# Optimization experiments

Measured on AMD Instinct MI355X. Metric: run time of the kernel, lower is better.

The kernel has to match this reference:

```python
import jax, jax.numpy as jnp
import numpy as np

B, V, H, NT, K_CD = 4096, 1024, 1024, 2, 10
L1_REG, L2_REG = 1e-5, 1e-4


def setup_inputs() -> dict:
    key = jax.random.key(0)
    ks = jax.random.split(key, 10)
    v0 = jax.random.bernoulli(ks[0], 0.5, (B, V)).astype(jnp.float32)
    # two distinct non-trivial (non-Z) sites per sample, one in each half
    tau0 = jax.random.randint(ks[1], (B,), 0, V // 2)
    tau1 = V // 2 + jax.random.randint(ks[2], (B,), 0, V // 2)
    tau_idx = jnp.stack([tau0, tau1], axis=1).astype(jnp.int32)
    basis_choice = jax.random.randint(ks[3], (B, NT), 1, 3).astype(jnp.int32)  # X=1 or Y=2
    basis_ids = jnp.zeros((B, V), jnp.int32)
    basis_ids = basis_ids.at[jnp.arange(B)[:, None], tau_idx].set(basis_choice)
    s = 1.0 / np.sqrt(2.0)
    un = np.zeros((3, 2, 2, 2), np.float32)  # [basis, row, col, re/im]
    un[0, :, :, 0] = np.eye(2)                              # Z: identity
    un[1, :, :, 0] = s * np.array([[1, 1], [1, -1]])        # X: Hadamard
    un[2, :, :, 0] = s * np.array([[1, 0], [1, 0]])         # Y: K gate, real
    un[2, :, :, 1] = s * np.array([[0, -1], [0, 1]])        # Y: K gate, imag
    unitaries = jnp.asarray(un)
    weights_amp = jax.random.normal(ks[4], (H, V), jnp.float32) / np.sqrt(V)
    weights_phase = 0.01 * jax.random.normal(ks[5], (H, V), jnp.float32)
    visible_bias_amp = 0.01 * jax.random.normal(ks[6], (V,), jnp.float32)
    hidden_bias_amp = 0.01 * jax.random.normal(ks[7], (H,), jnp.float32)
    visible_bias_phase = 0.01 * jax.random.normal(ks[8], (V,), jnp.float32)
    hidden_bias_phase = 0.01 * jax.random.normal(ks[9], (H,), jnp.float32)
    return {"v0": v0, "basis_ids": basis_ids, "tau_idx": tau_idx, "unitaries": unitaries,
            "weights_amp": weights_amp, "visible_bias_amp": visible_bias_amp,
            "hidden_bias_amp": hidden_bias_amp, "weights_phase": weights_phase,
            "visible_bias_phase": visible_bias_phase, "hidden_bias_phase": hidden_bias_phase,
            "k": K_CD}


def _forward(v0, unitaries, weights_amp, visible_bias_amp, hidden_bias_amp,
             weights_phase, visible_bias_phase, hidden_bias_phase,
             basis_ids, tau_idx, k):
    Bsz, Vn = v0.shape
    NTn = tau_idx.shape[1]
    C = 2 ** NTn
    # all 2^NT assignments of the rotated (tau) sites -> [C, NT]
    S = jnp.asarray(np.array([[(c >> (NTn - 1 - t)) & 1 for t in range(NTn)]
                              for c in range(C)], np.int32))
    U = (unitaries[..., 0] + 1j * unitaries[..., 1]).astype(jnp.complex64)  # [3,2,2]
    b_tau = jnp.take_along_axis(basis_ids, tau_idx, axis=1)                 # [B,NT]
    v0_tau = jnp.take_along_axis(v0, tau_idx, axis=1).astype(jnp.int32)     # [B,NT]
    # product over tau sites of unitary elements U_b[v0_j, s_j] -> [B,C]
    Uelem = U[b_tau[:, None, :], v0_tau[:, None, :], S[None, :, :]]
    wU = jnp.prod(Uelem, axis=-1)
    # v' = v0 with tau sites replaced by each assignment s -> [B,C,V]
    onehot = jax.nn.one_hot(tau_idx, Vn, dtype=v0.dtype)                    # [B,NT,V]
    mask = onehot.sum(1)
    vp = v0[:, None, :] * (1.0 - mask[:, None, :]) \
         + jnp.einsum('btv,ct->bcv', onehot, S.astype(v0.dtype))
    # unnormalized wavefunction psi(v') = sqrt(p_amp(v')) * exp(i*log(p_phase(v'))/2)
    pre_amp = jnp.einsum('bcv,hv->bch', vp, weights_amp) + hidden_bias_amp
    pre_ph = jnp.einsum('bcv,hv->bch', vp, weights_phase) + hidden_bias_phase
    log_amp = 0.5 * (vp @ visible_bias_amp + jax.nn.softplus(pre_amp).sum(-1))  # [B,C]
    theta = 0.5 * (vp @ visible_bias_phase + jax.nn.softplus(pre_ph).sum(-1))
    # per-sample shift cancels exactly in A/B; keeps exp() in fp32 range
    log_amp = log_amp - jax.lax.stop_gradient(log_amp.max(axis=1, keepdims=True))
    psi = (jnp.exp(log_amp) * (jnp.cos(theta) + 1j * jnp.sin(theta))).astype(jnp.complex64)
    w = wU * psi                                   # [B,C] complex
    coef = w / w.sum(axis=1, keepdims=True)        # A/B weighting per sample
    sig_amp = jax.nn.sigmoid(pre_amp)
    sig_ph = jax.nn.sigmoid(pre_ph)
    inv_b = 1.0 / Bsz
    Lw_amp = jnp.einsum('bc,bch,bcv->hv', coef, sig_amp, vp) * inv_b
    Lw_ph = jnp.einsum('bc,bch,bcv->hv', coef, sig_ph, vp) * inv_b
    Lvb = jnp.einsum('bc,bcv->v', coef, vp) * inv_b
    Lhb_amp = jnp.einsum('bc,bch->h', coef, sig_amp) * inv_b
    Lhb_ph = jnp.einsum('bc,bch->h', coef, sig_ph) * inv_b
    # amplitude params take Re(L) (negated positive phase); phase params take Im(L)
    g_w_amp = -jnp.real(Lw_amp)
    g_vb_amp = -jnp.real(Lvb)
    g_hb_amp = -jnp.real(Lhb_amp)
    g_w_ph = jnp.imag(Lw_ph)
    g_vb_ph = jnp.imag(Lvb)
    g_hb_ph = jnp.imag(Lhb_ph)
    # ---- CD-k Gibbs negative phase (amplitude RBM only) ----
    base_key = jax.random.key(1234)
    def gibbs_step(i, v):
        kh = jax.random.fold_in(base_key, 2 * i)
        kv = jax.random.fold_in(base_key, 2 * i + 1)
        ph = jax.nn.sigmoid(v @ weights_amp.T + hidden_bias_amp)
        h = (jax.random.uniform(kh, ph.shape) < ph).astype(v.dtype)
        pv = jax.nn.sigmoid(h @ weights_amp + visible_bias_amp)
        return (jax.random.uniform(kv, pv.shape) < pv).astype(v.dtype)
    vk = jax.lax.stop_gradient(jax.lax.fori_loop(0, k, gibbs_step, v0))
    sig_k = jax.nn.sigmoid(vk @ weights_amp.T + hidden_bias_amp)
    g_w_amp = g_w_amp + jnp.einsum('bh,bv->hv', sig_k, vk) * inv_b
    g_vb_amp = g_vb_amp + vk.mean(0)
    g_hb_amp = g_hb_amp + sig_k.mean(0)
    # ---- L1/L2 regularization on weight gradients ----
    g_w_amp = g_w_amp + L2_REG * weights_amp + L1_REG * jnp.sign(weights_amp)
    g_w_ph = g_w_ph + L2_REG * weights_phase + L1_REG * jnp.sign(weights_phase)
    return (g_w_amp, g_vb_amp, g_hb_amp, g_w_ph, g_vb_ph, g_hb_ph)


def reference(v0, basis_ids, tau_idx, unitaries, weights_amp, visible_bias_amp,
              hidden_bias_amp, weights_phase, visible_bias_phase, hidden_bias_phase, k):
    return _forward(v0, unitaries, weights_amp, visible_bias_amp, hidden_bias_amp,
                    weights_phase, visible_bias_phase, hidden_bias_phase,
                    basis_ids, tau_idx, k)
```

## Files before the change

### kernel.cpp

```cpp
#include <hip/hip_runtime.h>
#include <cstdint>
#include <cstddef>

#define BSZ 4096
#define VN  1024
#define HN  1024
#define NSTEPS 10

static constexpr float INVB = 1.0f / 4096.0f;
static constexpr float L1R  = 1e-5f;
static constexpr float L2R  = 1e-4f;

typedef __attribute__((ext_vector_type(8)))  __bf16        bf16x8;
typedef __attribute__((ext_vector_type(8)))  unsigned short ushort8;
typedef __attribute__((ext_vector_type(16))) float          f32x16;

__device__ static inline unsigned short f2bf(float x){
  unsigned u = __float_as_uint(x);
  unsigned r = (u + 0x7FFFu + ((u >> 16) & 1u)) >> 16;
  return (unsigned short)r;
}
__device__ static inline float bf2f(unsigned short s){
  return __uint_as_float(((unsigned)s) << 16);
}

__device__ __forceinline__ void gload16(const void* g, void* l){
  __builtin_amdgcn_global_load_lds(
      (__attribute__((address_space(1))) void*)(g),
      (__attribute__((address_space(3))) void*)(l),
      16, 0, 0);
}

#define TFR(x0,x1,r) { x0 += x1; x1 = ((x1)<<(r))|((x1)>>(32-(r))); x1 ^= x0; }

__host__ __device__ static inline void tf2x32(unsigned k0, unsigned k1,
                                              unsigned x0, unsigned x1,
                                              unsigned &o0, unsigned &o1)
{
  const unsigned ks2 = k0 ^ k1 ^ 0x1BD11BDAu;
  x0 += k0; x1 += k1;
  TFR(x0,x1,13) TFR(x0,x1,15) TFR(x0,x1,26) TFR(x0,x1,6)
  x0 += k1; x1 += ks2 + 1u;
  TFR(x0,x1,17) TFR(x0,x1,29) TFR(x0,x1,16) TFR(x0,x1,24)
  x0 += ks2; x1 += k0 + 2u;
  TFR(x0,x1,13) TFR(x0,x1,15) TFR(x0,x1,26) TFR(x0,x1,6)
  x0 += k0; x1 += k1 + 3u;
  TFR(x0,x1,17) TFR(x0,x1,29) TFR(x0,x1,16) TFR(x0,x1,24)
  x0 += k1; x1 += ks2 + 4u;
  TFR(x0,x1,13) TFR(x0,x1,15) TFR(x0,x1,26) TFR(x0,x1,6)
  x0 += ks2; x1 += k0 + 5u;
  o0 = x0; o1 = x1;
}

__device__ static inline float tf_uniform(unsigned k0, unsigned k1, unsigned e)
{
  unsigned o0, o1; tf2x32(k0, k1, 0u, e, o0, o1);
  const unsigned r = o0 ^ o1;
  return __uint_as_float((r >> 9) | 0x3f800000u) - 1.0f;
}

__device__ static inline float sigmoidf(float x){ return 1.0f/(1.0f+expf(-x)); }

__global__ void zero_kernel(float* __restrict__ p, int n){
  int i = blockIdx.x*256 + threadIdx.x;
  if (i < n) p[i] = 0.0f;
}

__global__ void prep_kernel(const float* __restrict__ v0,
                            const int* __restrict__ tau,
                            float* __restrict__ v0m,
                            float* __restrict__ v_cur,
                            unsigned short* __restrict__ v0m_bf,
                            unsigned short* __restrict__ v_bf)
{
  int i = blockIdx.x*256 + threadIdx.x;
  int b = i >> 10;
  int v = i & (VN-1);
  float x = v0[i];
  v_cur[i] = x;
  v_bf[i]  = f2bf(x);
  int t0 = tau[2*b], t1 = tau[2*b+1];
  float xm = (v==t0 || v==t1) ? 0.0f : x;
  v0m[i]    = xm;
  v0m_bf[i] = f2bf(xm);
}

__global__ void transpose_kernel(const float* __restrict__ Wa,
                                 const float* __restrict__ Wp,
                                 float* __restrict__ WTa,
                                 float* __restrict__ WTp)
{
  __shared__ float tile[32][33];
  const float* in = blockIdx.z ? Wp : Wa;
  float* out      = blockIdx.z ? WTp : WTa;
  int x  = blockIdx.x*32 + threadIdx.x;
  int y0 = blockIdx.y*32;
  for (int j = threadIdx.y; j < 32; j += 8)
    tile[j][threadIdx.x] = in[(size_t)(y0+j)*VN + x];
  __syncthreads();
  int xo  = y0 + threadIdx.x;
  int yo0 = blockIdx.x*32;
  for (int j = threadIdx.y; j < 32; j += 8)
    out[(size_t)(yo0+j)*HN + xo] = tile[threadIdx.x][j];
}

__global__ void transpose_to_bf(const float* __restrict__ X,
                                unsigned short* __restrict__ XT,
                                float* __restrict__ cs)
{
  __shared__ float tile[32][33];
  const int tx = threadIdx.x, ty = threadIdx.y;
  int x  = blockIdx.x*32 + tx;
  int y0 = blockIdx.y*32;
  for (int j = ty; j < 32; j += 8)
    tile[j][tx] = X[(size_t)(y0+j)*1024 + x];
  __syncthreads();
  int xo  = y0 + tx;
  int yo0 = blockIdx.x*32;
  for (int j = ty; j < 32; j += 8)
    XT[(size_t)(yo0+j)*BSZ + xo] = f2bf(tile[tx][j]);
  float s = tile[ty][tx] + tile[ty+8][tx] + tile[ty+16][tx] + tile[ty+24][tx];
  __syncthreads();
  tile[ty][tx] = s;
  __syncthreads();
  if (ty == 0){
    float t = 0.f;
    #pragma unroll
    for (int j = 0; j < 8; j++) t += tile[j][tx];
    atomicAdd(cs + x, t);
  }
}

__global__ void split_weights(const float* __restrict__ Wa,
                              const float* __restrict__ Wp,
                              const float* __restrict__ WTa,
                              unsigned short* __restrict__ WaHi,
                              unsigned short* __restrict__ WaLo,
                              unsigned short* __restrict__ WpHi,
                              unsigned short* __restrict__ WpLo,
                              unsigned short* __restrict__ WaTHi,
                              unsigned short* __restrict__ WaTLo)
{
  size_t i = (size_t)blockIdx.x*256 + threadIdx.x;
  float w = Wa[i];  unsigned short h = f2bf(w);
  WaHi[i] = h;  WaLo[i] = f2bf(w - bf2f(h));
  w = Wp[i];  h = f2bf(w);
  WpHi[i] = h;  WpLo[i] = f2bf(w - bf2f(h));
  w = WTa[i]; h = f2bf(w);
  WaTHi[i] = h; WaTLo[i] = f2bf(w - bf2f(h));
}

#define GM 64
#define GN 64
#define GK 64

template<int MODE>
__global__ __launch_bounds__(256) void mfma_nt(
    const unsigned short* __restrict__ A,
    const unsigned short* __restrict__ Bhi,
    const unsigned short* __restrict__ Blo,
    const float* __restrict__ bias,
    unsigned short* __restrict__ out_bf,
    float* __restrict__ out_f,
    unsigned key0, unsigned key1)
{
  constexpr int K = 1024;
  constexpr int N = 1024;
  __shared__ ushort8 ldsA [GM*8];
  __shared__ ushort8 ldsBh[GN*8];
  __shared__ ushort8 ldsBl[GN*8];

  const int orig = blockIdx.x + gridDim.x * blockIdx.y;
  const int swz  = (orig & 7) * 128 + (orig >> 3);
  const int bx   = swz & 15, by = swz >> 4;
  const int m0   = by*GM, n0 = bx*GN;

  const int tid  = threadIdx.x;
  const int lane = tid & 63, w = tid >> 6;
  const int wm = w >> 1, wn = w & 1;
  const int l31 = lane & 31, hi = lane >> 5;
  const int rsub = lane >> 3;
  const int cch  = lane & 7;

  f32x16 acc = {};

  const int arow = wm*32 + l31;
  const int brow = wn*32 + l31;
  const int aswz = arow & 7;
  const int bswz = brow & 7;
  const int aidx = arow*8;
  const int bidx = brow*8;

  for (int kt = 0; kt < K/GK; ++kt){
    __syncthreads();
    const size_t kbase = (size_t)kt*GK;
    #pragma unroll
    for (int p = 0; p < 2; p++){
      const int row  = p*32 + w*8 + rsub;
      const int csrc = cch ^ (row & 7);
      gload16(A   + (size_t)(m0+row)*K + kbase + csrc*8, &ldsA [(p*32 + w*8)*8]);
      gload16(Bhi + (size_t)(n0+row)*K + kbase + csrc*8, &ldsBh[(p*32 + w*8)*8]);
      gload16(Blo + (size_t)(n0+row)*K + kbase + csrc*8, &ldsBl[(p*32 + w*8)*8]);
    }
    __syncthreads();

    #pragma unroll
    for (int s = 0; s < 4; s++){
      const int c = s*2 + hi;
      const bf16x8 a  = __builtin_bit_cast(bf16x8, ldsA [aidx + (c ^ aswz)]);
      const bf16x8 bh = __builtin_bit_cast(bf16x8, ldsBh[bidx + (c ^ bswz)]);
      const bf16x8 bl = __builtin_bit_cast(bf16x8, ldsBl[bidx + (c ^ bswz)]);
      acc = __builtin_amdgcn_mfma_f32_32x32x16_bf16(a, bh, acc, 0, 0, 0);
      acc = __builtin_amdgcn_mfma_f32_32x32x16_bf16(a, bl, acc, 0, 0, 0);
    }
  }

  const int n  = n0 + wn*32 + l31;
  const float bv = bias[n];
  const int mbase = m0 + wm*32 + 4*hi;
  #pragma unroll
  for (int r = 0; r < 16; r++){
    const int m = mbase + (r&3) + 8*(r>>2);
    const float pre = acc[r] + bv;
    const size_t o = (size_t)m*N + n;
    if constexpr (MODE == 0 || MODE == 1){
      const float p = sigmoidf(pre);
      const float u = tf_uniform(key0, key1, (unsigned)(m*N + n));
      out_bf[o] = (u < p) ? (unsigned short)0x3F80 : (unsigned short)0;
      if constexpr (MODE == 1) out_f[o] = (u < p) ? 1.0f : 0.0f;
    } else if constexpr (MODE == 2){
      out_f[o] = sigmoidf(pre);
    } else {
      out_f[o] = pre;
    }
  }
}

template<int NPROD>
__global__ __launch_bounds__(256) void mfma_grad(
    const unsigned short* __restrict__ A1,
    const unsigned short* __restrict__ B1,
    const unsigned short* __restrict__ A2,
    const unsigned short* __restrict__ B2,
    const float* __restrict__ Wreg,
    float* __restrict__ gW)
{
  constexpr int K = BSZ;
  __shared__ ushort8 lA1[64*8];
  __shared__ ushort8 lB1[64*8];
  __shared__ ushort8 lA2[(NPROD==2)?64*8:1];
  __shared__ ushort8 lB2[(NPROD==2)?64*8:1];

  const int tid  = threadIdx.x;
  const int m0   = blockIdx.y*64, n0 = blockIdx.x*64;
  const int lane = tid & 63, w = tid >> 6;
  const int wm = w >> 1, wn = w & 1;
  const int l31 = lane & 31, hi = lane >> 5;
  const int srow = tid >> 3, sc = tid & 7;

  f32x16 acc1a = {}, acc1b = {}, acc2a = {}, acc2b = {};

  const int arow = wm*32 + l31;
  const int brow = wn*32 + l31;
  const int aswz = arow & 7, bswz = brow & 7;
  const int aidx = arow*8,  bidx = brow*8;

  for (int kt = 0; kt < K/64; ++kt){
    __syncthreads();
    const size_t kof = (size_t)kt*64 + sc*8;
    #pragma unroll
    for (int p = 0; p < 2; p++){
      const int row = p*32 + srow;
      const int c = sc ^ (row & 7);
      lA1[row*8 + c] = *(const ushort8*)(A1 + (size_t)(m0+row)*K + kof);
      lB1[row*8 + c] = *(const ushort8*)(B1 + (size_t)(n0+row)*K + kof);
      if constexpr (NPROD==2){
        lA2[row*8 + c] = *(const ushort8*)(A2 + (size_t)(m0+row)*K + kof);
        lB2[row*8 + c] = *(const ushort8*)(B2 + (size_t)(n0+row)*K + kof);
      }
    }
    __syncthreads();
    #pragma unroll
    for (int s = 0; s < 4; s++){
      const int c = s*2 + hi;
      const bf16x8 a1 = __builtin_bit_cast(bf16x8, lA1[aidx + (c ^ aswz)]);
      const bf16x8 b1 = __builtin_bit_cast(bf16x8, lB1[bidx + (c ^ bswz)]);
      if (s & 1) acc1b = __builtin_amdgcn_mfma_f32_32x32x16_bf16(a1, b1, acc1b, 0,0,0);
      else       acc1a = __builtin_amdgcn_mfma_f32_32x32x16_bf16(a1, b1, acc1a, 0,0,0);
      if constexpr (NPROD==2){
        const bf16x8 a2 = __builtin_bit_cast(bf16x8, lA2[aidx + (c ^ aswz)]);
        const bf16x8 b2 = __builtin_bit_cast(bf16x8, lB2[bidx + (c ^ bswz)]);
        if (s & 1) acc2b = __builtin_amdgcn_mfma_f32_32x32x16_bf16(a2, b2, acc2b, 0,0,0);
        else       acc2a = __builtin_amdgcn_mfma_f32_32x32x16_bf16(a2, b2, acc2a, 0,0,0);
      }
    }
  }

  const int n = n0 + wn*32 + l31;
  #pragma unroll
  for (int r = 0; r < 16; r++){
    const int m = m0 + wm*32 + 4*hi + (r&3) + 8*(r>>2);
    const size_t o = (size_t)m*VN + n;
    float val;
    if constexpr (NPROD==2)
      val = INVB*((acc1a[r]+acc1b[r]) - (acc2a[r]+acc2b[r]));
    else
      val = INVB*(acc1a[r]+acc1b[r]);
    const float wv = Wreg[o];
    const float sg = (wv>0.f)?1.f:((wv<0.f)?-1.f:0.f);
    gW[o] += val + L2R*wv + L1R*sg;
  }
}

__global__ __launch_bounds__(256) void coef_ramp_kernel(
    const float* __restrict__ pre0a, const float* __restrict__ pre0p,
    const float* __restrict__ WTa,   const float* __restrict__ WTp,
    const float* __restrict__ v0,
    const float* __restrict__ vbA,   const float* __restrict__ vbP,
    const int*   __restrict__ tau,   const int*   __restrict__ basis,
    const float* __restrict__ unit,
    float* __restrict__ coefRe, float* __restrict__ coefIm,
    float* __restrict__ tmpA,   float* __restrict__ tmpP,
    float* __restrict__ Ramp,   float* __restrict__ Iph)
{
  const int b = blockIdx.x;
  const int t = threadIdx.x;
  const int t0 = tau[2*b], t1 = tau[2*b+1];

  float d[6] = {0,0,0,0,0,0};
  float st_sa[4], st_sp[4], st_a0[4], st_a1[4], st_p0[4], st_p1[4];

  #pragma unroll
  for (int i = 0; i < 4; i++){
    const int h = t + i*256;
    const float pa = pre0a[(size_t)b*HN + h], pp = pre0p[(size_t)b*HN + h];
    const float a0 = WTa[(size_t)t0*HN + h], a1 = WTa[(size_t)t1*HN + h];
    const float p0 = WTp[(size_t)t0*HN + h], p1 = WTp[(size_t)t1*HN + h];
    const float sa  = sigmoidf(pa);
    const float sp  = sigmoidf(pp);
    const float s1a = sa*(1.f-sa), ta2 = 1.f-2.f*sa, s2a = s1a*ta2;
    const float s1p = sp*(1.f-sp), tp2 = 1.f-2.f*sp, s2p = s1p*tp2;
    const float a01 = a0 + a1, p01 = p0 + p1;
    d[0] += a1 *(sa + a1 *(0.5f*s1a + 0.16666667f*a1 *s2a));
    d[1] += a0 *(sa + a0 *(0.5f*s1a + 0.16666667f*a0 *s2a));
    d[2] += a01*(sa + a01*(0.5f*s1a + 0.16666667f*a01*s2a));
    d[3] += p1 *(sp + p1 *(0.5f*s1p + 0.16666667f*p1 *s2p));
    d[4] += p0 *(sp + p0 *(0.5f*s1p + 0.16666667f*p0 *s2p));
    d[5] += p01*(sp + p01*(0.5f*s1p + 0.16666667f*p01*s2p));
    st_sa[i]=sa; st_sp[i]=sp; st_a0[i]=a0; st_a1[i]=a1; st_p0[i]=p0; st_p1[i]=p1;
  }

  __shared__ float red[6][4];
  __shared__ float lcr[4], lci[4];
  const int lane = t & 63, wv = t >> 6;
  #pragma unroll
  for (int i=0;i<6;i++){
    float x = d[i];
    for (int off=32; off>0; off>>=1) x += __shfl_down(x, off);
    if (lane==0) red[i][wv] = x;
  }
  __syncthreads();

  if (t==0){
    double ds[6];
    #pragma unroll
    for (int i=0;i<6;i++)
      ds[i] = (double)red[i][0]+red[i][1]+red[i][2]+red[i][3];

    const int bas0 = basis[(size_t)b*VN + t0], bas1 = basis[(size_t)b*VN + t1];
    const int x0 = (int)v0[(size_t)b*VN + t0], x1 = (int)v0[(size_t)b*VN + t1];
    const double A0 = vbA[t0], A1 = vbA[t1], P0 = vbP[t0], P1 = vbP[t1];

    double la[4], th[4];
    la[0]=0.0;                th[0]=0.0;
    la[1]=0.5*(A1+ds[0]);     th[1]=0.5*(P1+ds[3]);
    la[2]=0.5*(A0+ds[1]);     th[2]=0.5*(P0+ds[4]);
    la[3]=0.5*(A0+A1+ds[2]);  th[3]=0.5*(P0+P1+ds[5]);

    double wR[4], wI[4], sr=0.0, si=0.0;
    #pragma unroll
    for (int c=0;c<4;c++){
      const int s0 = (c>>1)&1, s1 = c&1;
      const float* u0 = unit + (((size_t)bas0*2 + x0)*2 + s0)*2;
      const float* u1 = unit + (((size_t)bas1*2 + x1)*2 + s1)*2;
      const double uR = (double)u0[0]*u1[0] - (double)u0[1]*u1[1];
      const double uI = (double)u0[0]*u1[1] + (double)u0[1]*u1[0];
      const double e  = exp(la[c]);
      const double cs = cos(th[c]), sn = sin(th[c]);
      wR[c] = e*(uR*cs - uI*sn);
      wI[c] = e*(uR*sn + uI*cs);
      sr += wR[c]; si += wI[c];
    }
    const double dd = sr*sr + si*si;
    #pragma unroll
    for (int c=0;c<4;c++){
      const float cr = (float)((wR[c]*sr + wI[c]*si)/dd);
      const float ci = (float)((wI[c]*sr - wR[c]*si)/dd);
      coefRe[b*4+c] = cr;  coefIm[b*4+c] = ci;
      lcr[c] = cr;         lci[c] = ci;
    }
    atomicAdd(tmpA + t0, lcr[2]+lcr[3]);
    atomicAdd(tmpA + t1, lcr[1]+lcr[3]);
    atomicAdd(tmpP + t0, lci[2]+lci[3]);
    atomicAdd(tmpP + t1, lci[1]+lci[3]);
  }
  __syncthreads();

  const float cr0=lcr[0], cr1=lcr[1], cr2=lcr[2], cr3=lcr[3];
  const float ci0=lci[0], ci1=lci[1], ci2=lci[2], ci3=lci[3];

  #pragma unroll
  for (int i = 0; i < 4; i++){
    const int h = t + i*256;
    const float sa = st_sa[i], sp = st_sp[i];
    const float a0 = st_a0[i], a1 = st_a1[i], p0 = st_p0[i], p1 = st_p1[i];
    const float s1a = sa*(1.f-sa), ta2 = 1.f-2.f*sa;
    const float s2a = s1a*ta2,     s3a = s1a*(ta2*ta2 - 2.f*s1a);
    const float s1p = sp*(1.f-sp), tp2 = 1.f-2.f*sp;
    const float s2p = s1p*tp2,     s3p = s1p*(tp2*tp2 - 2.f*s1p);
    const float a01 = a0 + a1, p01 = p0 + p1;
    const float sgA1 = sa + a1 *(s1a + a1 *(0.5f*s2a + 0.16666667f*a1 *s3a));
    const float sgA0 = sa + a0 *(s1a + a0 *(0.5f*s2a + 0.16666667f*a0 *s3a));
    const float sgA01= sa + a01*(s1a + a01*(0.5f*s2a + 0.16666667f*a01*s3a));
    const float sgP1 = sp + p1 *(s1p + p1 *(0.5f*s2p + 0.16666667f*p1 *s3p));
    const float sgP0 = sp + p0 *(s1p + p0 *(0.5f*s2p + 0.16666667f*p0 *s3p));
    const float sgP01= sp + p01*(s1p + p01*(0.5f*s2p + 0.16666667f*p01*s3p));
    Ramp[(size_t)b*HN + h] = cr0*sa + cr1*sgA1 + cr2*sgA0 + cr3*sgA01;
    Iph [(size_t)b*HN + h] = ci0*sp + ci1*sgP1 + ci2*sgP0 + ci3*sgP01;
  }
}

__global__ void csr_count(const int* __restrict__ tau, int* __restrict__ cnt){
  int b = blockIdx.x*256 + threadIdx.x;
  atomicAdd(cnt + tau[2*b],   1);
  atomicAdd(cnt + tau[2*b+1], 1);
}

__global__ __launch_bounds__(1024) void csr_scan(const int* __restrict__ cnt,
                                                 int* __restrict__ off,
                                                 int* __restrict__ cur){
  __shared__ int s[1024];
  const int t = threadIdx.x;
  s[t] = cnt[t];
  __syncthreads();
  for (int d=1; d<1024; d<<=1){
    int v = 0;
    if (t >= d) v = s[t-d];
    __syncthreads();
    s[t] += v;
    __syncthreads();
  }
  const int excl = (t==0) ? 0 : s[t-1];
  off[t] = excl; cur[t] = excl;
}

__global__ void csr_fill(const int* __restrict__ tau, int* __restrict__ cur,
                         int* __restrict__ list){
  int b = blockIdx.x*256 + threadIdx.x;
  int p0 = atomicAdd(cur + tau[2*b],   1); list[p0] = b;
  int p1 = atomicAdd(cur + tau[2*b+1], 1); list[p1] = b;
}

__global__ __launch_bounds__(256) void scatter_v2(
    const float* __restrict__ pre0a, const float* __restrict__ pre0p,
    const float* __restrict__ WTa,   const float* __restrict__ WTp,
    const int*   __restrict__ tau,
    const float* __restrict__ coefRe, const float* __restrict__ coefIm,
    const int* __restrict__ cnt, const int* __restrict__ off,
    const int* __restrict__ list,
    float* __restrict__ gWa, float* __restrict__ gWp)
{
  const int v = blockIdx.x;
  const int n = cnt[v];
  if (n == 0) return;
  const int o = off[v];
  const int c_lo = (v < 512) ? 2 : 1;
  const bool lo_half = (v < 512);

  const int h = blockIdx.y*256 + threadIdx.x;
  const float av = WTa[(size_t)v*HN + h];
  const float pv = WTp[(size_t)v*HN + h];
  float accA = 0.f, accP = 0.f;
  int e = o;
  for (; e + 2 <= o + n; e += 2){
    const int b0 = list[e], b1 = list[e+1];
    const int ot0 = lo_half ? tau[2*b0+1] : tau[2*b0];
    const int ot1 = lo_half ? tau[2*b1+1] : tau[2*b1];
    const float aoA0 = WTa[(size_t)ot0*HN + h], aoA1 = WTa[(size_t)ot1*HN + h];
    const float aoP0 = WTp[(size_t)ot0*HN + h], aoP1 = WTp[(size_t)ot1*HN + h];
    const float pa0 = pre0a[(size_t)b0*HN + h], pa1 = pre0a[(size_t)b1*HN + h];
    const float pp0 = pre0p[(size_t)b0*HN + h], pp1 = pre0p[(size_t)b1*HN + h];
    const float crl0 = coefRe[b0*4 + c_lo], cr30 = coefRe[b0*4 + 3];
    const float cil0 = coefIm[b0*4 + c_lo], ci30 = coefIm[b0*4 + 3];
    const float crl1 = coefRe[b1*4 + c_lo], cr31 = coefRe[b1*4 + 3];
    const float cil1 = coefIm[b1*4 + c_lo], ci31 = coefIm[b1*4 + 3];
    accA += crl0*sigmoidf(pa0 + av) + cr30*sigmoidf(pa0 + av + aoA0);
    accP += cil0*sigmoidf(pp0 + pv) + ci30*sigmoidf(pp0 + pv + aoP0);
    accA += crl1*sigmoidf(pa1 + av) + cr31*sigmoidf(pa1 + av + aoA1);
    accP += cil1*sigmoidf(pp1 + pv) + ci31*sigmoidf(pp1 + pv + aoP1);
  }
  if (e < o + n){
    const int b0 = list[e];
    const int ot0 = lo_half ? tau[2*b0+1] : tau[2*b0];
    const float aoA0 = WTa[(size_t)ot0*HN + h];
    const float aoP0 = WTp[(size_t)ot0*HN + h];
    const float pa0 = pre0a[(size_t)b0*HN + h];
    const float pp0 = pre0p[(size_t)b0*HN + h];
    const float crl0 = coefRe[b0*4 + c_lo], cr30 = coefRe[b0*4 + 3];
    const float cil0 = coefIm[b0*4 + c_lo], ci30 = coefIm[b0*4 + 3];
    accA += crl0*sigmoidf(pa0 + av) + cr30*sigmoidf(pa0 + av + aoA0);
    accP += cil0*sigmoidf(pp0 + pv) + ci30*sigmoidf(pp0 + pv + aoP0);
  }
  gWa[(size_t)h*VN + v] += -INVB*accA;
  gWp[(size_t)h*VN + v] +=  INVB*accP;
}

__global__ void final_small(
    const float* __restrict__ csV0m, const float* __restrict__ csVk,
    const float* __restrict__ csSigk, const float* __restrict__ csRamp,
    const float* __restrict__ csIph,
    const float* __restrict__ tmpA, const float* __restrict__ tmpP,
    float* __restrict__ gVa, float* __restrict__ gHa,
    float* __restrict__ gVp, float* __restrict__ gHp)
{
  const int j = blockIdx.x*256 + threadIdx.x;
  if (j < VN){
    gVa[j] = INVB*(csVk[j] - csV0m[j] - tmpA[j]);
    gVp[j] = INVB*tmpP[j];
  }
  if (j < HN){
    gHa[j] = INVB*(csSigk[j] - csRamp[j]);
    gHp[j] = INVB*csIph[j];
  }
}

extern "C" void kernel_launch(void* const* d_in, const int* in_sizes, int n_in,
                              void* d_out, int out_size, void* d_ws, size_t ws_size,
                              hipStream_t stream)
{
  const float* v0    = (const float*)d_in[0];
  const int*   basis = (const int*)  d_in[1];
  const int*   tau   = (const int*)  d_in[2];
  const float* unit  = (const float*)d_in[3];
  const float* Wa    = (const float*)d_in[4];
  const float* vbA   = (const float*)d_in[5];
  const float* hbA   = (const float*)d_in[6];
  const float* Wp    = (const float*)d_in[7];
  const float* vbP   = (const float*)d_in[8];
  const float* hbP   = (const float*)d_in[9];

  float* ws    = (float*)d_ws;
  float* v0m   = ws;  ws += (size_t)BSZ*VN;
  float* v_cur = ws;  ws += (size_t)BSZ*VN;
  float* h_buf = ws;  ws += (size_t)BSZ*HN;
  float* WTa   = ws;  ws += (size_t)VN*HN;
  float* WTp   = ws;  ws += (size_t)VN*HN;
  float* pre0a = ws;  ws += (size_t)BSZ*HN;
  float* pre0p = ws;  ws += (size_t)BSZ*HN;
  float* Ramp  = ws;  ws += (size_t)BSZ*HN;
  float* Iph   = ws;  ws += (size_t)BSZ*HN;
  float* coefRe= ws;  ws += (size_t)BSZ*4;
  float* coefIm= ws;  ws += (size_t)BSZ*4;
  float* tmpA  = ws;  ws += VN;
  float* tmpP  = ws;  ws += VN;
  float* csV0m = ws;  ws += VN;
  float* csVk  = ws;  ws += VN;
  float* csSigk= ws;  ws += HN;
  float* csRamp= ws;  ws += HN;
  float* csIph = ws;  ws += HN;
  int*   csrCnt = (int*)ws;  ws += VN;
  int*   csrOff = (int*)ws;  ws += VN;
  int*   csrCur = (int*)ws;  ws += VN;
  int*   csrLst = (int*)ws;  ws += 2*BSZ;
  unsigned short* v_bf    = (unsigned short*)ws;  ws += (size_t)BSZ*VN/2;
  unsigned short* h_bf    = (unsigned short*)ws;  ws += (size_t)BSZ*HN/2;
  unsigned short* v0m_bf  = (unsigned short*)ws;  ws += (size_t)BSZ*VN/2;
  unsigned short* WaHi    = (unsigned short*)ws;  ws += (size_t)HN*VN/2;
  unsigned short* WaLo    = (unsigned short*)ws;  ws += (size_t)HN*VN/2;
  unsigned short* WpHi    = (unsigned short*)ws;  ws += (size_t)HN*VN/2;
  unsigned short* WpLo    = (unsigned short*)ws;  ws += (size_t)HN*VN/2;
  unsigned short* WaTHi   = (unsigned short*)ws;  ws += (size_t)HN*VN/2;
  unsigned short* WaTLo   = (unsigned short*)ws;  ws += (size_t)HN*VN/2;

  float* sig_k = h_buf;
  unsigned short* v0mT  = (unsigned short*)pre0a;
  unsigned short* vkT   = v0mT + (size_t)VN*BSZ;
  unsigned short* RampT = (unsigned short*)pre0p;
  unsigned short* IphT  = RampT + (size_t)HN*BSZ;
  unsigned short* sigkT = (unsigned short*)WTa;

  float* out = (float*)d_out;
  float* gWa = out;
  float* gVa = gWa + (size_t)HN*VN;
  float* gHa = gVa + VN;
  float* gWp = gHa + HN;
  float* gVp = gWp + (size_t)HN*VN;
  float* gHp = gVp + VN;

  const dim3 gemm_grid(VN/GN, BSZ/GM);
  const dim3 tr_grid(1024/32, BSZ/32);
  const dim3 tr_blk(32, 8);

  zero_kernel<<<dim3(40), 256, 0, stream>>>(tmpA, 10*1024);
  zero_kernel<<<dim3((out_size+255)/256), 256, 0, stream>>>(out, out_size);
  prep_kernel<<<dim3(BSZ*VN/256), 256, 0, stream>>>(v0, tau, v0m, v_cur, v0m_bf, v_bf);
  transpose_kernel<<<dim3(VN/32, HN/32, 2), dim3(32,8), 0, stream>>>(Wa, Wp, WTa, WTp);
  split_weights<<<dim3(HN*VN/256), 256, 0, stream>>>(
      Wa, Wp, WTa, WaHi, WaLo, WpHi, WpLo, WaTHi, WaTLo);

  mfma_nt<3><<<gemm_grid, 256, 0, stream>>>(
      v0m_bf, WaHi, WaLo, hbA, nullptr, pre0a, 0u, 0u);
  mfma_nt<3><<<gemm_grid, 256, 0, stream>>>(
      v0m_bf, WpHi, WpLo, hbP, nullptr, pre0p, 0u, 0u);
  coef_ramp_kernel<<<dim3(BSZ), 256, 0, stream>>>(
      pre0a, pre0p, WTa, WTp, v0, vbA, vbP, tau, basis, unit,
      coefRe, coefIm, tmpA, tmpP, Ramp, Iph);

  csr_count<<<dim3(BSZ/256), 256, 0, stream>>>(tau, csrCnt);
  csr_scan <<<dim3(1), 1024, 0, stream>>>(csrCnt, csrOff, csrCur);
  csr_fill <<<dim3(BSZ/256), 256, 0, stream>>>(tau, csrCur, csrLst);
  scatter_v2<<<dim3(VN, 4), 256, 0, stream>>>(
      pre0a, pre0p, WTa, WTp, tau, coefRe, coefIm,
      csrCnt, csrOff, csrLst, gWa, gWp);

  for (int i = 0; i < NSTEPS; i++){
    unsigned kh0, kh1, kv0, kv1;
    tf2x32(0u, 1234u, 0u, (unsigned)(2*i),   kh0, kh1);
    tf2x32(0u, 1234u, 0u, (unsigned)(2*i+1), kv0, kv1);
    mfma_nt<0><<<gemm_grid, 256, 0, stream>>>(
        v_bf, WaHi, WaLo, hbA, h_bf, nullptr, kh0, kh1);
    if (i < NSTEPS-1)
      mfma_nt<0><<<gemm_grid, 256, 0, stream>>>(
          h_bf, WaTHi, WaTLo, vbA, v_bf, nullptr, kv0, kv1);
    else
      mfma_nt<1><<<gemm_grid, 256, 0, stream>>>(
          h_bf, WaTHi, WaTLo, vbA, v_bf, v_cur, kv0, kv1);
  }
  mfma_nt<2><<<gemm_grid, 256, 0, stream>>>(
      v_bf, WaHi, WaLo, hbA, nullptr, sig_k, 0u, 0u);

  transpose_to_bf<<<tr_grid, tr_blk, 0, stream>>>(v0m,   v0mT,  csV0m);
  transpose_to_bf<<<tr_grid, tr_blk, 0, stream>>>(v_cur, vkT,   csVk);
  transpose_to_bf<<<tr_grid, tr_blk, 0, stream>>>(Ramp,  RampT, csRamp);
  transpose_to_bf<<<tr_grid, tr_blk, 0, stream>>>(Iph,   IphT,  csIph);
  transpose_to_bf<<<tr_grid, tr_blk, 0, stream>>>(sig_k, sigkT, csSigk);

  mfma_grad<2><<<dim3(VN/64, HN/64), 256, 0, stream>>>(
      sigkT, vkT, RampT, v0mT, Wa, gWa);
  mfma_grad<1><<<dim3(VN/64, HN/64), 256, 0, stream>>>(
      IphT, v0mT, nullptr, nullptr, Wp, gWp);

  final_small<<<dim3(4), 256, 0, stream>>>(
      csV0m, csVk, csSigk, csRamp, csIph, tmpA, tmpP, gVa, gHa, gVp, gHp);
}
```

Measured before the change: 965.4 us.

## Enlarge Gibbs GEMM tiles to 128x128 with 2x2 MFMA blocking per wave

The forward GEMM kernel's block tile grows from 64x64 to 128x128. Each wave now computes a 64x64 sub-tile with four 32x32 accumulators, so every A and B fragment read from LDS is reused twice. The grid swizzle and epilogue loops are rewritten to match the larger tile. The aim is to cut global and LDS traffic per FLOP in the Gibbs sampling GEMMs. The costs are fewer blocks (256 instead of 1024), which can hurt occupancy and load balance, plus higher register pressure from 64 accumulator floats per lane.

```diff
diff --git a/kernel.cpp b/kernel.cpp
--- a/kernel.cpp
+++ b/kernel.cpp
@@ -150,8 +150,8 @@
   WaTHi[i] = h; WaTLo[i] = f2bf(w - bf2f(h));
 }
 
-#define GM 64
-#define GN 64
+#define GM 128
+#define GN 128
 #define GK 64
 
 template<int MODE>
@@ -171,8 +171,8 @@
   __shared__ ushort8 ldsBl[GN*8];
 
   const int orig = blockIdx.x + gridDim.x * blockIdx.y;
-  const int swz  = (orig & 7) * 128 + (orig >> 3);
-  const int bx   = swz & 15, by = swz >> 4;
+  const int swz  = (orig & 7) * 32 + (orig >> 3);
+  const int bx   = swz & 7, by = swz >> 3;
   const int m0   = by*GM, n0 = bx*GN;
 
   const int tid  = threadIdx.x;
@@ -182,20 +182,20 @@
   const int rsub = lane >> 3;
   const int cch  = lane & 7;
 
-  f32x16 acc = {};
-
-  const int arow = wm*32 + l31;
-  const int brow = wn*32 + l31;
-  const int aswz = arow & 7;
-  const int bswz = brow & 7;
-  const int aidx = arow*8;
-  const int bidx = brow*8;
+  f32x16 acc00 = {}, acc01 = {}, acc10 = {}, acc11 = {};
+
+  const int arow0 = wm*64 + l31;
+  const int brow0 = wn*64 + l31;
+  const int aswz  = arow0 & 7;
+  const int bswz  = brow0 & 7;
+  const int aidx0 = arow0*8,      aidx1 = (arow0+32)*8;
+  const int bidx0 = brow0*8,      bidx1 = (brow0+32)*8;
 
   for (int kt = 0; kt < K/GK; ++kt){
     __syncthreads();
     const size_t kbase = (size_t)kt*GK;
     #pragma unroll
-    for (int p = 0; p < 2; p++){
+    for (int p = 0; p < 4; p++){
       const int row  = p*32 + w*8 + rsub;
       const int csrc = cch ^ (row & 7);
       gload16(A   + (size_t)(m0+row)*K + kbase + csrc*8, &ldsA [(p*32 + w*8)*8]);
@@ -207,31 +207,47 @@
     #pragma unroll
     for (int s = 0; s < 4; s++){
       const int c = s*2 + hi;
-      const bf16x8 a  = __builtin_bit_cast(bf16x8, ldsA [aidx + (c ^ aswz)]);
-      const bf16x8 bh = __builtin_bit_cast(bf16x8, ldsBh[bidx + (c ^ bswz)]);
-      const bf16x8 bl = __builtin_bit_cast(bf16x8, ldsBl[bidx + (c ^ bswz)]);
-      acc = __builtin_amdgcn_mfma_f32_32x32x16_bf16(a, bh, acc, 0, 0, 0);
-      acc = __builtin_amdgcn_mfma_f32_32x32x16_bf16(a, bl, acc, 0, 0, 0);
+      const bf16x8 a0  = __builtin_bit_cast(bf16x8, ldsA [aidx0 + (c ^ aswz)]);
+      const bf16x8 a1  = __builtin_bit_cast(bf16x8, ldsA [aidx1 + (c ^ aswz)]);
+      const bf16x8 bh0 = __builtin_bit_cast(bf16x8, ldsBh[bidx0 + (c ^ bswz)]);
+      const bf16x8 bl0 = __builtin_bit_cast(bf16x8, ldsBl[bidx0 + (c ^ bswz)]);
+      const bf16x8 bh1 = __builtin_bit_cast(bf16x8, ldsBh[bidx1 + (c ^ bswz)]);
+      const bf16x8 bl1 = __builtin_bit_cast(bf16x8, ldsBl[bidx1 + (c ^ bswz)]);
+      acc00 = __builtin_amdgcn_mfma_f32_32x32x16_bf16(a0, bh0, acc00, 0, 0, 0);
+      acc00 = __builtin_amdgcn_mfma_f32_32x32x16_bf16(a0, bl0, acc00, 0, 0, 0);
+      acc01 = __builtin_amdgcn_mfma_f32_32x32x16_bf16(a0, bh1, acc01, 0, 0, 0);
+      acc01 = __builtin_amdgcn_mfma_f32_32x32x16_bf16(a0, bl1, acc01, 0, 0, 0);
+      acc10 = __builtin_amdgcn_mfma_f32_32x32x16_bf16(a1, bh0, acc10, 0, 0, 0);
+      acc10 = __builtin_amdgcn_mfma_f32_32x32x16_bf16(a1, bl0, acc10, 0, 0, 0);
+      acc11 = __builtin_amdgcn_mfma_f32_32x32x16_bf16(a1, bh1, acc11, 0, 0, 0);
+      acc11 = __builtin_amdgcn_mfma_f32_32x32x16_bf16(a1, bl1, acc11, 0, 0, 0);
     }
   }
 
-  const int n  = n0 + wn*32 + l31;
-  const float bv = bias[n];
-  const int mbase = m0 + wm*32 + 4*hi;
   #pragma unroll
-  for (int r = 0; r < 16; r++){
-    const int m = mbase + (r&3) + 8*(r>>2);
-    const float pre = acc[r] + bv;
-    const size_t o = (size_t)m*N + n;
-    if constexpr (MODE == 0 || MODE == 1){
-      const float p = sigmoidf(pre);
-      const float u = tf_uniform(key0, key1, (unsigned)(m*N + n));
-      out_bf[o] = (u < p) ? (unsigned short)0x3F80 : (unsigned short)0;
-      if constexpr (MODE == 1) out_f[o] = (u < p) ? 1.0f : 0.0f;
-    } else if constexpr (MODE == 2){
-      out_f[o] = sigmoidf(pre);
-    } else {
-      out_f[o] = pre;
+  for (int ai = 0; ai < 2; ai++){
+    #pragma unroll
+    for (int bj = 0; bj < 2; bj++){
+      const f32x16 acc = ai ? (bj ? acc11 : acc10) : (bj ? acc01 : acc00);
+      const int n  = n0 + wn*64 + bj*32 + l31;
+      const float bv = bias[n];
+      const int mbase = m0 + wm*64 + ai*32 + 4*hi;
+      #pragma unroll
+      for (int r = 0; r < 16; r++){
+        const int m = mbase + (r&3) + 8*(r>>2);
+        const float pre = acc[r] + bv;
+        const size_t o = (size_t)m*N + n;
+        if constexpr (MODE == 0 || MODE == 1){
+          const float p = sigmoidf(pre);
+          const float u = tf_uniform(key0, key1, (unsigned)(m*N + n));
+          out_bf[o] = (u < p) ? (unsigned short)0x3F80 : (unsigned short)0;
+          if constexpr (MODE == 1) out_f[o] = (u < p) ? 1.0f : 0.0f;
+        } else if constexpr (MODE == 2){
+          out_f[o] = sigmoidf(pre);
+        } else {
+          out_f[o] = pre;
+        }
+      }
     }
   }
 }
```

New measurement: 1.142 ms. 1.18x slower.

## Rewrite tau-site scatter with bf16 operands, coalesced staging and transpose-add

Applied to the files above, without the earlier changes.

The scatter kernel now reads bf16 copies of the pre-activations and transposed weights, which the forward GEMM epilogue and split_weights produce. Each thread handles four hidden units with vector loads and writes a dense [V,H] staging buffer with coalesced stores. A new tiled transpose kernel then writes the weight-gradient outputs, so the strided read-modify-write into the output and the output zeroing launch go away. The cost is reduced precision in the scatter term, because bf16 pre-activations and weights replace fp32, plus extra bf16 writes during the GEMMs.

```diff
diff --git a/kernel.cpp b/kernel.cpp
--- a/kernel.cpp
+++ b/kernel.cpp
@@ -13,6 +13,8 @@
 
 typedef __attribute__((ext_vector_type(8)))  __bf16        bf16x8;
 typedef __attribute__((ext_vector_type(8)))  unsigned short ushort8;
+typedef __attribute__((ext_vector_type(4)))  unsigned short ushort4v;
+typedef __attribute__((ext_vector_type(4)))  float          f32x4;
 typedef __attribute__((ext_vector_type(16))) float          f32x16;
 
 __device__ static inline unsigned short f2bf(float x){
@@ -134,12 +136,14 @@
 __global__ void split_weights(const float* __restrict__ Wa,
                               const float* __restrict__ Wp,
                               const float* __restrict__ WTa,
+                              const float* __restrict__ WTp,
                               unsigned short* __restrict__ WaHi,
                               unsigned short* __restrict__ WaLo,
                               unsigned short* __restrict__ WpHi,
                               unsigned short* __restrict__ WpLo,
                               unsigned short* __restrict__ WaTHi,
-                              unsigned short* __restrict__ WaTLo)
+                              unsigned short* __restrict__ WaTLo,
+                              unsigned short* __restrict__ WpTHi)
 {
   size_t i = (size_t)blockIdx.x*256 + threadIdx.x;
   float w = Wa[i];  unsigned short h = f2bf(w);
@@ -148,6 +152,7 @@
   WpHi[i] = h;  WpLo[i] = f2bf(w - bf2f(h));
   w = WTa[i]; h = f2bf(w);
   WaTHi[i] = h; WaTLo[i] = f2bf(w - bf2f(h));
+  WpTHi[i] = f2bf(WTp[i]);
 }
 
 #define GM 64
@@ -231,7 +236,8 @@
     } else if constexpr (MODE == 2){
       out_f[o] = sigmoidf(pre);
     } else {
-      out_f[o] = pre;
+      out_f[o]  = pre;
+      out_bf[o] = f2bf(pre);
     }
   }
 }
@@ -461,58 +467,73 @@
   int p1 = atomicAdd(cur + tau[2*b+1], 1); list[p1] = b;
 }
 
-__global__ __launch_bounds__(256) void scatter_v2(
-    const float* __restrict__ pre0a, const float* __restrict__ pre0p,
-    const float* __restrict__ WTa,   const float* __restrict__ WTp,
+__global__ __launch_bounds__(256) void scatter_v3(
+    const unsigned short* __restrict__ pre0aBF,
+    const unsigned short* __restrict__ pre0pBF,
+    const unsigned short* __restrict__ WaTHi,
+    const unsigned short* __restrict__ WpTHi,
     const int*   __restrict__ tau,
     const float* __restrict__ coefRe, const float* __restrict__ coefIm,
     const int* __restrict__ cnt, const int* __restrict__ off,
     const int* __restrict__ list,
-    float* __restrict__ gWa, float* __restrict__ gWp)
-{
-  const int v = blockIdx.x;
-  const int n = cnt[v];
-  if (n == 0) return;
-  const int o = off[v];
+    float* __restrict__ gSa, float* __restrict__ gSp)
+{
+  const int v  = blockIdx.x;
+  const int h0 = threadIdx.x * 4;
+  const int n  = cnt[v];
+  const int o  = off[v];
   const int c_lo = (v < 512) ? 2 : 1;
   const bool lo_half = (v < 512);
 
-  const int h = blockIdx.y*256 + threadIdx.x;
-  const float av = WTa[(size_t)v*HN + h];
-  const float pv = WTp[(size_t)v*HN + h];
-  float accA = 0.f, accP = 0.f;
-  int e = o;
-  for (; e + 2 <= o + n; e += 2){
-    const int b0 = list[e], b1 = list[e+1];
-    const int ot0 = lo_half ? tau[2*b0+1] : tau[2*b0];
-    const int ot1 = lo_half ? tau[2*b1+1] : tau[2*b1];
-    const float aoA0 = WTa[(size_t)ot0*HN + h], aoA1 = WTa[(size_t)ot1*HN + h];
-    const float aoP0 = WTp[(size_t)ot0*HN + h], aoP1 = WTp[(size_t)ot1*HN + h];
-    const float pa0 = pre0a[(size_t)b0*HN + h], pa1 = pre0a[(size_t)b1*HN + h];
-    const float pp0 = pre0p[(size_t)b0*HN + h], pp1 = pre0p[(size_t)b1*HN + h];
-    const float crl0 = coefRe[b0*4 + c_lo], cr30 = coefRe[b0*4 + 3];
-    const float cil0 = coefIm[b0*4 + c_lo], ci30 = coefIm[b0*4 + 3];
-    const float crl1 = coefRe[b1*4 + c_lo], cr31 = coefRe[b1*4 + 3];
-    const float cil1 = coefIm[b1*4 + c_lo], ci31 = coefIm[b1*4 + 3];
-    accA += crl0*sigmoidf(pa0 + av) + cr30*sigmoidf(pa0 + av + aoA0);
-    accP += cil0*sigmoidf(pp0 + pv) + ci30*sigmoidf(pp0 + pv + aoP0);
-    accA += crl1*sigmoidf(pa1 + av) + cr31*sigmoidf(pa1 + av + aoA1);
-    accP += cil1*sigmoidf(pp1 + pv) + ci31*sigmoidf(pp1 + pv + aoP1);
-  }
-  if (e < o + n){
-    const int b0 = list[e];
-    const int ot0 = lo_half ? tau[2*b0+1] : tau[2*b0];
-    const float aoA0 = WTa[(size_t)ot0*HN + h];
-    const float aoP0 = WTp[(size_t)ot0*HN + h];
-    const float pa0 = pre0a[(size_t)b0*HN + h];
-    const float pp0 = pre0p[(size_t)b0*HN + h];
-    const float crl0 = coefRe[b0*4 + c_lo], cr30 = coefRe[b0*4 + 3];
-    const float cil0 = coefIm[b0*4 + c_lo], ci30 = coefIm[b0*4 + 3];
-    accA += crl0*sigmoidf(pa0 + av) + cr30*sigmoidf(pa0 + av + aoA0);
-    accP += cil0*sigmoidf(pp0 + pv) + ci30*sigmoidf(pp0 + pv + aoP0);
-  }
-  gWa[(size_t)h*VN + v] += -INVB*accA;
-  gWp[(size_t)h*VN + v] +=  INVB*accP;
+  float accA[4] = {0,0,0,0}, accP[4] = {0,0,0,0};
+  if (n > 0){
+    const ushort4v avu = *(const ushort4v*)(WaTHi + (size_t)v*HN + h0);
+    const ushort4v pvu = *(const ushort4v*)(WpTHi + (size_t)v*HN + h0);
+    float av[4], pv[4];
+    #pragma unroll
+    for (int j=0;j<4;j++){ av[j]=bf2f(avu[j]); pv[j]=bf2f(pvu[j]); }
+    for (int e = o; e < o + n; e++){
+      const int b  = list[e];
+      const int ot = lo_half ? tau[2*b+1] : tau[2*b];
+      const ushort4v ao = *(const ushort4v*)(WaTHi  + (size_t)ot*HN + h0);
+      const ushort4v po = *(const ushort4v*)(WpTHi  + (size_t)ot*HN + h0);
+      const ushort4v pa = *(const ushort4v*)(pre0aBF + (size_t)b*HN + h0);
+      const ushort4v pp = *(const ushort4v*)(pre0pBF + (size_t)b*HN + h0);
+      const float crl = coefRe[b*4 + c_lo], cr3 = coefRe[b*4 + 3];
+      const float cil = coefIm[b*4 + c_lo], ci3 = coefIm[b*4 + 3];
+      #pragma unroll
+      for (int j=0;j<4;j++){
+        const float paf = bf2f(pa[j]) + av[j];
+        const float ppf = bf2f(pp[j]) + pv[j];
+        accA[j] += crl*sigmoidf(paf) + cr3*sigmoidf(paf + bf2f(ao[j]));
+        accP[j] += cil*sigmoidf(ppf) + ci3*sigmoidf(ppf + bf2f(po[j]));
+      }
+    }
+  }
+  f32x4 ra, rp;
+  #pragma unroll
+  for (int j=0;j<4;j++){ ra[j]=accA[j]; rp[j]=accP[j]; }
+  *(f32x4*)(gSa + (size_t)v*HN + h0) = ra;
+  *(f32x4*)(gSp + (size_t)v*HN + h0) = rp;
+}
+
+__global__ void tadd_kernel(const float* __restrict__ gSa,
+                            const float* __restrict__ gSp,
+                            float* __restrict__ gWa,
+                            float* __restrict__ gWp)
+{
+  __shared__ float ta[32][33], tp[32][33];
+  const int tx = threadIdx.x, ty = threadIdx.y;
+  const int v0 = blockIdx.x*32, h0 = blockIdx.y*32;
+  for (int j = ty; j < 32; j += 8){
+    ta[j][tx] = gSa[(size_t)(v0+j)*HN + h0 + tx];
+    tp[j][tx] = gSp[(size_t)(v0+j)*HN + h0 + tx];
+  }
+  __syncthreads();
+  for (int j = ty; j < 32; j += 8){
+    gWa[(size_t)(h0+j)*VN + v0 + tx] = -INVB*ta[tx][j];
+    gWp[(size_t)(h0+j)*VN + v0 + tx] =  INVB*tp[tx][j];
+  }
 }
 
 __global__ void final_small(
@@ -581,8 +602,13 @@
   unsigned short* WpLo    = (unsigned short*)ws;  ws += (size_t)HN*VN/2;
   unsigned short* WaTHi   = (unsigned short*)ws;  ws += (size_t)HN*VN/2;
   unsigned short* WaTLo   = (unsigned short*)ws;  ws += (size_t)HN*VN/2;
+  unsigned short* WpTHi   = (unsigned short*)ws;  ws += (size_t)HN*VN/2;
 
   float* sig_k = h_buf;
+  unsigned short* pre0aBF = (unsigned short*)h_buf;
+  unsigned short* pre0pBF = pre0aBF + (size_t)BSZ*HN;
+  float* gSa = pre0a;
+  float* gSp = pre0a + (size_t)VN*HN;
   unsigned short* v0mT  = (unsigned short*)pre0a;
   unsigned short* vkT   = v0mT + (size_t)VN*BSZ;
   unsigned short* RampT = (unsigned short*)pre0p;
@@ -602,16 +628,15 @@
   const dim3 tr_blk(32, 8);
 
   zero_kernel<<<dim3(40), 256, 0, stream>>>(tmpA, 10*1024);
-  zero_kernel<<<dim3((out_size+255)/256), 256, 0, stream>>>(out, out_size);
   prep_kernel<<<dim3(BSZ*VN/256), 256, 0, stream>>>(v0, tau, v0m, v_cur, v0m_bf, v_bf);
   transpose_kernel<<<dim3(VN/32, HN/32, 2), dim3(32,8), 0, stream>>>(Wa, Wp, WTa, WTp);
   split_weights<<<dim3(HN*VN/256), 256, 0, stream>>>(
-      Wa, Wp, WTa, WaHi, WaLo, WpHi, WpLo, WaTHi, WaTLo);
+      Wa, Wp, WTa, WTp, WaHi, WaLo, WpHi, WpLo, WaTHi, WaTLo, WpTHi);
 
   mfma_nt<3><<<gemm_grid, 256, 0, stream>>>(
-      v0m_bf, WaHi, WaLo, hbA, nullptr, pre0a, 0u, 0u);
+      v0m_bf, WaHi, WaLo, hbA, pre0aBF, pre0a, 0u, 0u);
   mfma_nt<3><<<gemm_grid, 256, 0, stream>>>(
-      v0m_bf, WpHi, WpLo, hbP, nullptr, pre0p, 0u, 0u);
+      v0m_bf, WpHi, WpLo, hbP, pre0pBF, pre0p, 0u, 0u);
   coef_ramp_kernel<<<dim3(BSZ), 256, 0, stream>>>(
       pre0a, pre0p, WTa, WTp, v0, vbA, vbP, tau, basis, unit,
       coefRe, coefIm, tmpA, tmpP, Ramp, Iph);
@@ -619,9 +644,11 @@
   csr_count<<<dim3(BSZ/256), 256, 0, stream>>>(tau, csrCnt);
   csr_scan <<<dim3(1), 1024, 0, stream>>>(csrCnt, csrOff, csrCur);
   csr_fill <<<dim3(BSZ/256), 256, 0, stream>>>(tau, csrCur, csrLst);
-  scatter_v2<<<dim3(VN, 4), 256, 0, stream>>>(
-      pre0a, pre0p, WTa, WTp, tau, coefRe, coefIm,
-      csrCnt, csrOff, csrLst, gWa, gWp);
+  scatter_v3<<<dim3(VN), 256, 0, stream>>>(
+      pre0aBF, pre0pBF, WaTHi, WpTHi, tau, coefRe, coefIm,
+      csrCnt, csrOff, csrLst, gSa, gSp);
+  tadd_kernel<<<dim3(VN/32, HN/32), dim3(32,8), 0, stream>>>(
+      gSa, gSp, gWa, gWp);
 
   for (int i = 0; i < NSTEPS; i++){
     unsigned kh0, kh1, kv0, kv1;
```

Result: faster. 935.8 us (-3.1%).
